# Performance work log

Hardware: AMD Instinct MI355X
Metric: run time of the kernel (lower is better)

Reference implementation:

```python
import jax, jax.numpy as jnp
import numpy as np

B, H, V, T = 32768, 1024, 9, 20
EOS = 8

def setup_inputs() -> dict:
    key = jax.random.key(0)
    ks = jax.random.split(key, 10)
    s_fc = 1.0 / np.sqrt(784)
    s_ih = 1.0 / np.sqrt(V)
    s_hh = 1.0 / np.sqrt(H)
    u = jax.random.uniform(ks[9], (T, B, V), jnp.float32, 1e-10, 1.0)
    return {
        "x": jax.random.normal(ks[0], (B, 784), jnp.float32),
        "tau": jnp.float32(1.0),
        "fc_w": jax.random.normal(ks[1], (H, 784), jnp.float32) * s_fc,
        "w_ih": jax.random.normal(ks[2], (3 * H, V), jnp.float32) * s_ih,
        "w_hh": jax.random.normal(ks[3], (3 * H, H), jnp.float32) * s_hh,
        "b_ih": jax.random.normal(ks[4], (3 * H,), jnp.float32) * s_hh,
        "b_hh": jax.random.normal(ks[5], (3 * H,), jnp.float32) * s_hh,
        "proj_w": jax.random.normal(ks[6], (V, H), jnp.float32) * s_hh,
        "proj_b": jax.random.normal(ks[7], (V,), jnp.float32) * s_hh,
        # standard Gumbel(0,1) noise, precomputed for all T steps
        "gumbel": -jnp.log(-jnp.log(u)),
    }


def reference(x, tau, fc_w, w_ih, w_hh, b_ih, b_hh, proj_w, proj_b, gumbel):
    # context = gelu(fc(x)); dropout is identity (eval mode)
    h0 = jax.nn.gelu(x @ fc_w.T, approximate=False)  # [B, H]
    b = x.shape[0]
    tok0 = jnp.zeros((b, V), x.dtype).at[:, 0].set(1.0)  # BOS one-hot

    def step(carry, g):
        h, tok, finished, lengths, t = carry
        gi = tok @ w_ih.T + b_ih            # [B, 3H]
        gh = h @ w_hh.T + b_hh              # [B, 3H]
        i_r, i_z, i_n = jnp.split(gi, 3, axis=-1)
        h_r, h_z, h_n = jnp.split(gh, 3, axis=-1)
        r = jax.nn.sigmoid(i_r + h_r)
        z = jax.nn.sigmoid(i_z + h_z)
        n = jnp.tanh(i_n + r * h_n)
        h_new = (1.0 - z) * n + z * h
        logits = h_new @ proj_w.T + proj_b  # [B, V]
        y_soft = jax.nn.softmax((logits + g) / tau, axis=-1)
        idx = jnp.argmax(y_soft, axis=-1)
        y_hard = jax.nn.one_hot(idx, V, dtype=y_soft.dtype)
        y = y_hard + y_soft - jax.lax.stop_gradient(y_soft)  # straight-through
        newly = (idx == EOS) & (~finished)
        lengths = jnp.where(newly, t + 1, lengths)
        finished = finished | newly
        return (h_new, y, finished, lengths, t + 1), y

    carry0 = (h0, tok0,
              jnp.zeros((b,), jnp.bool_),
              jnp.full((b,), T, jnp.int32),
              jnp.int32(0))
    (_, _, _, lengths, _), toks = jax.lax.scan(step, carry0, gumbel)
    message = jnp.transpose(toks, (1, 0, 2))  # [B, T, V]
    return message, lengths
```

## Files before the change

kernel.cpp:

```cpp
#include <hip/hip_runtime.h>
#include <math.h>

#define Bsz 32768
#define Hd  1024
#define Vn  9
#define Tn  20
#define EOSv 8
#define KFC 784
#define PLANE 33554432ull

typedef float f4 __attribute__((ext_vector_type(4)));
typedef float f32x16 __attribute__((ext_vector_type(16)));
typedef _Float16 h8 __attribute__((ext_vector_type(8)));
typedef unsigned short us4 __attribute__((ext_vector_type(4)));
typedef unsigned short us8v __attribute__((ext_vector_type(8)));

__device__ __forceinline__ unsigned short f16_rne(float x) {
    _Float16 h = (_Float16)x;
    return __builtin_bit_cast(unsigned short, h);
}
__device__ __forceinline__ float f16_val(unsigned short u) {
    return (float)__builtin_bit_cast(_Float16, u);
}
__device__ __forceinline__ void split2h(float x, unsigned short& p0, unsigned short& p1) {
    p0 = f16_rne(x);
    float r = x - f16_val(p0);
    p1 = f16_rne(r);
}
__device__ __forceinline__ int slotr(int r) { return r ^ ((r >> 3) & 3); }

__device__ __forceinline__ void gload16(const void* g, void* l) {
    __builtin_amdgcn_global_load_lds(
        (const __attribute__((address_space(1))) unsigned int*)g,
        (__attribute__((address_space(3))) unsigned int*)l, 16, 0, 0);
}

__global__ __launch_bounds__(256) void k_init(int* __restrict__ st,
                                              float* __restrict__ lenf) {
    int i = blockIdx.x * 256 + threadIdx.x;
    if (i < Bsz) { st[i] = 0; lenf[i] = (float)Tn; }
}

__global__ __launch_bounds__(256) void k_prep(const float* __restrict__ wih,
                                              const float* __restrict__ bih,
                                              float* __restrict__ giTab) {
    int i = blockIdx.x * 256 + threadIdx.x;
    int tk = i / 3072, n = i - tk * 3072;
    giTab[i] = wih[(size_t)n * Vn + tk] + bih[n];
}

__global__ __launch_bounds__(256) void k_prepB(const float* __restrict__ whh,
                                               unsigned short* __restrict__ wp) {
    int g = blockIdx.x * 256 + threadIdx.x;
    int lane = g & 63, u = g >> 6;
    int p = u & 1, kc = (u >> 1) & 63, ct = u >> 7;
    int col = ct * 32 + (lane & 31);
    int k = kc * 16 + (lane >> 5) * 8;
    const float* src = whh + (size_t)col * Hd + k;
    unsigned short v[8];
    #pragma unroll
    for (int i = 0; i < 8; ++i) {
        unsigned short s0, s1; split2h(src[i], s0, s1);
        v[i] = (p == 0) ? s0 : s1;
    }
    unsigned short* dst = wp + (size_t)u * 512 + lane * 8;
    us4 w0; w0[0]=v[0]; w0[1]=v[1]; w0[2]=v[2]; w0[3]=v[3];
    us4 w1; w1[0]=v[4]; w1[1]=v[5]; w1[2]=v[6]; w1[3]=v[7];
    *(us4*)dst = w0;
    *(us4*)(dst + 4) = w1;
}

__global__ __launch_bounds__(256) void k_fcP(const float* __restrict__ x,
                                             const float* __restrict__ fcw,
                                             float* __restrict__ h0,
                                             unsigned short* __restrict__ hp) {
    __shared__ float As[16][68];
    __shared__ float Ws[16][68];
    const int tid = threadIdx.x;
    const int tx = tid & 15, ty = tid >> 4;
    const int m0 = blockIdx.x * 64, n0 = blockIdx.y * 64;
    const int lrow = tid >> 2, lkc = (tid & 3) << 2;
    float acc[4][4] = {};
    for (int k0 = 0; k0 < KFC; k0 += 16) {
        f4 a = *(const f4*)(x   + (size_t)(m0 + lrow) * KFC + k0 + lkc);
        f4 w = *(const f4*)(fcw + (size_t)(n0 + lrow) * KFC + k0 + lkc);
        #pragma unroll
        for (int q = 0; q < 4; ++q) { As[lkc + q][lrow] = a[q]; Ws[lkc + q][lrow] = w[q]; }
        __syncthreads();
        #pragma unroll
        for (int kk = 0; kk < 16; ++kk) {
            f4 av = *(const f4*)&As[kk][ty * 4];
            f4 wv = *(const f4*)&Ws[kk][tx * 4];
            #pragma unroll
            for (int i = 0; i < 4; ++i)
                #pragma unroll
                for (int j = 0; j < 4; ++j)
                    acc[i][j] = fmaf(av[i], wv[j], acc[i][j]);
        }
        __syncthreads();
    }
    #pragma unroll
    for (int i = 0; i < 4; ++i) {
        int b = m0 + ty * 4 + i;
        int cb = n0 + tx * 4;
        f4 hv;
        us4 q0, q1;
        #pragma unroll
        for (int j = 0; j < 4; ++j) {
            float v = acc[i][j];
            float gl = 0.5f * v * (1.0f + erff(v * 0.70710678118654752f));
            hv[j] = gl;
            unsigned short s0, s1; split2h(gl, s0, s1);
            q0[j] = s0; q1[j] = s1;
        }
        *(f4*)&h0[(size_t)b * Hd + cb] = hv;
        *(us4*)&hp[0 * PLANE + (size_t)b * Hd + cb] = q0;
        *(us4*)&hp[1 * PLANE + (size_t)b * Hd + cb] = q1;
    }
}

__global__ __launch_bounds__(256, 3) void k_step(
        const unsigned short* __restrict__ hp, float* __restrict__ h,
        const unsigned short* __restrict__ wp, const float* __restrict__ bhh,
        const float* __restrict__ giTab, const int* __restrict__ st) {
    __shared__ unsigned short Asm[2][2 * 2 * 128 * 8];
    __shared__ unsigned short Bsm[2][12 * 512];
    const int tid = threadIdx.x;
    const int lane = tid & 63, wid = tid >> 6;
    const int wm = wid >> 1, wn = wid & 1;
    const int l31 = lane & 31, lh = lane >> 5;

    const int w = blockIdx.x;
    const int cg = (w & 7) * 2 + ((w >> 3) & 1);
    const int rb = w >> 4;
    const int m_blk = rb * 128;
    const int c0 = cg * 64;

    f32x16 acc[2][3];
    #pragma unroll
    for (int mt = 0; mt < 2; ++mt)
        #pragma unroll
        for (int g = 0; g < 3; ++g)
            #pragma unroll
            for (int e = 0; e < 16; ++e) acc[mt][g][e] = 0.0f;

    const int ar = tid >> 1;
    const int kh = tid & 1;
    const int wslot = slotr(ar);
    int rslot[2];
    #pragma unroll
    for (int mt = 0; mt < 2; ++mt) rslot[mt] = slotr(wm * 64 + mt * 32 + l31);

    us8v pa[2];
    auto load_a = [&](int s) {
        const size_t base = (size_t)(m_blk + ar) * Hd + (s << 4) + (kh << 3);
        pa[0] = *(const us8v*)&hp[0 * PLANE + base];
        pa[1] = *(const us8v*)&hp[1 * PLANE + base];
    };
    auto write_a = [&](int bufi) {
        *(us8v*)&Asm[bufi][((0 * 2 + kh) * 128 + wslot) * 8] = pa[0];
        *(us8v*)&Asm[bufi][((1 * 2 + kh) * 128 + wslot) * 8] = pa[1];
    };
    auto stage_b = [&](int s, int bufi) {
        #pragma unroll
        for (int q = 0; q < 3; ++q) {
            const int u = wid * 3 + q;
            const int ctl = u >> 1, p = u & 1;
            const int g = ctl >> 1, wnl = ctl & 1;
            const int ct = g * 32 + cg * 2 + wnl;
            const unsigned short* src = wp + ((size_t)(ct * 64 + s) * 2 + p) * 512 + lane * 8;
            gload16(src, &Bsm[bufi][u * 512]);
        }
    };

    stage_b(0, 0);
    load_a(0);
    write_a(0);
    load_a(1);
    __syncthreads();

    for (int s = 0; s < 64; ++s) {
        const int bi = s & 1;
        if (s < 63) {
            stage_b(s + 1, bi ^ 1);
            write_a(bi ^ 1);
        }
        if (s < 62) load_a(s + 2);
        h8 af[2][2];
        #pragma unroll
        for (int mt = 0; mt < 2; ++mt)
            #pragma unroll
            for (int p = 0; p < 2; ++p)
                af[mt][p] = *(const h8*)&Asm[bi][((p * 2 + lh) * 128 + rslot[mt]) * 8];
        #pragma unroll
        for (int g = 0; g < 3; ++g) {
            const int ub = (g * 2 + wn) * 2;
            h8 b0 = *(const h8*)&Bsm[bi][(ub + 0) * 512 + lane * 8];
            h8 b1 = *(const h8*)&Bsm[bi][(ub + 1) * 512 + lane * 8];
            #pragma unroll
            for (int mt = 0; mt < 2; ++mt) {
                f32x16 c = acc[mt][g];
                c = __builtin_amdgcn_mfma_f32_32x32x16_f16(af[mt][0], b1, c, 0, 0, 0);
                c = __builtin_amdgcn_mfma_f32_32x32x16_f16(af[mt][1], b0, c, 0, 0, 0);
                c = __builtin_amdgcn_mfma_f32_32x32x16_f16(af[mt][0], b0, c, 0, 0, 0);
                acc[mt][g] = c;
            }
        }
        __syncthreads();
    }

    const int col = c0 + wn * 32 + l31;
    const float bhr = bhh[col], bhz = bhh[Hd + col], bhn = bhh[2 * Hd + col];
    #pragma unroll
    for (int mt = 0; mt < 2; ++mt) {
        #pragma unroll
        for (int reg = 0; reg < 16; ++reg) {
            const int row = m_blk + wm * 64 + mt * 32 + 4 * lh + (reg & 3) + 8 * (reg >> 2);
            const int tk = st[row] & 15;
            const float* gi = giTab + tk * 3072;
            float rr = 1.0f / (1.0f + expf(-(gi[col] + acc[mt][0][reg] + bhr)));
            float zz = 1.0f / (1.0f + expf(-(gi[Hd + col] + acc[mt][1][reg] + bhz)));
            float nn = tanhf(gi[2 * Hd + col] + rr * (acc[mt][2][reg] + bhn));
            const size_t off = (size_t)row * Hd + col;
            float hold = h[off];
            h[off] = (1.0f - zz) * nn + zz * hold;
        }
    }
}

__global__ __launch_bounds__(256) void k_projP(const float* __restrict__ hnew,
        unsigned short* __restrict__ hp,
        const float* __restrict__ pw, const float* __restrict__ pb,
        const float* __restrict__ gum, const float* __restrict__ tau,
        float* __restrict__ msg, float* __restrict__ lenf,
        int* __restrict__ st, int t) {
    const int lane = threadIdx.x & 63;
    const int wv = threadIdx.x >> 6;
    const int b = blockIdx.x * 4 + wv;
    const float* hr = hnew + (size_t)b * Hd;
    float s[Vn] = {};
    float vals[16];
    #pragma unroll
    for (int c0 = 0; c0 < 16; c0 += 4) {
        f4 hv = *(const f4*)(hr + lane * 16 + c0);
        #pragma unroll
        for (int q = 0; q < 4; ++q) vals[c0 + q] = hv[q];
        #pragma unroll
        for (int v = 0; v < Vn; ++v) {
            f4 pv = *(const f4*)(pw + (size_t)v * Hd + lane * 16 + c0);
            #pragma unroll
            for (int q = 0; q < 4; ++q) s[v] = fmaf(hv[q], pv[q], s[v]);
        }
    }
    us8v o0[2], o1[2];
    #pragma unroll
    for (int hh = 0; hh < 2; ++hh)
        #pragma unroll
        for (int e = 0; e < 8; ++e) {
            unsigned short q0, q1;
            split2h(vals[hh * 8 + e], q0, q1);
            o0[hh][e] = q0; o1[hh][e] = q1;
        }
    size_t base = (size_t)b * Hd + lane * 16;
    #pragma unroll
    for (int hh = 0; hh < 2; ++hh) {
        *(us8v*)&hp[0 * PLANE + base + hh * 8] = o0[hh];
        *(us8v*)&hp[1 * PLANE + base + hh * 8] = o1[hh];
    }
    #pragma unroll
    for (int v = 0; v < Vn; ++v)
        #pragma unroll
        for (int off = 32; off > 0; off >>= 1)
            s[v] += __shfl_xor(s[v], off, 64);
    if (lane == 0) {
        const float tv = tau[0];
        float zv[Vn];
        #pragma unroll
        for (int v = 0; v < Vn; ++v)
            zv[v] = (s[v] + pb[v] + gum[(size_t)b * Vn + v]) / tv;
        int idx = 0; float m = zv[0];
        #pragma unroll
        for (int v = 1; v < Vn; ++v)
            if (zv[v] > m) { m = zv[v]; idx = v; }
        float* orow = msg + ((size_t)b * Tn + t) * Vn;
        #pragma unroll
        for (int v = 0; v < Vn; ++v) orow[v] = (v == idx) ? 1.0f : 0.0f;
        const int old = st[b];
        const int fn = old >> 4;
        st[b] = idx | (((fn != 0) || (idx == EOSv)) ? 16 : 0);
        if (idx == EOSv && fn == 0) lenf[b] = (float)(t + 1);
    }
}

extern "C" void kernel_launch(void* const* d_in, const int* in_sizes, int n_in,
                              void* d_out, int out_size, void* d_ws, size_t ws_size,
                              hipStream_t stream) {
    const float* x   = (const float*)d_in[0];
    const float* tau = (const float*)d_in[1];
    const float* fcw = (const float*)d_in[2];
    const float* wih = (const float*)d_in[3];
    const float* whh = (const float*)d_in[4];
    const float* bih = (const float*)d_in[5];
    const float* bhh = (const float*)d_in[6];
    const float* pw  = (const float*)d_in[7];
    const float* pb  = (const float*)d_in[8];
    const float* gum = (const float*)d_in[9];

    float* msg  = (float*)d_out;
    float* lenf = msg + (size_t)Bsz * Tn * Vn;

    char* ws = (char*)d_ws;
    float*          h     = (float*)ws;
    unsigned short* hp    = (unsigned short*)(ws + 134217728ull);
    unsigned short* wpb   = (unsigned short*)(ws + 268435456ull);
    float*          giTab = (float*)(ws + 281018368ull);
    int*            st    = (int*)  (ws + 281128960ull);

    k_init<<<Bsz / 256, 256, 0, stream>>>(st, lenf);
    k_prep<<<108, 256, 0, stream>>>(wih, bih, giTab);
    k_prepB<<<3072, 256, 0, stream>>>(whh, wpb);
    k_fcP<<<dim3(Bsz / 64, Hd / 64), 256, 0, stream>>>(x, fcw, h, hp);
    for (int t = 0; t < Tn; ++t) {
        k_step<<<4096, 256, 0, stream>>>(hp, h, wpb, bhh, giTab, st);
        k_projP<<<Bsz / 4, 256, 0, stream>>>(h, hp, pw, pb,
                                             gum + (size_t)t * Bsz * Vn,
                                             tau, msg, lenf, st, t);
    }
}
```

Baseline: 17.44 ms.

## Reshape GRU step tile to 64x128 with eight waves per block

Changes the recurrent GEMM block tile from 128 rows by 64 columns with four waves to 64 rows by 128 columns with eight waves, each wave holding one 32-row tile across three gates. This halves how many column groups re-read each h row from global memory, reducing activation traffic, while doubling weight staging per block. It also lowers per-wave accumulator registers but reduces MFMA work per shared-memory fragment load, and only half the threads load A.

```diff
diff --git a/kernel.cpp b/kernel.cpp
--- a/kernel.cpp
+++ b/kernel.cpp
@@ -119,92 +119,79 @@
     }
 }
 
-__global__ __launch_bounds__(256, 3) void k_step(
+__global__ __launch_bounds__(512) void k_step(
         const unsigned short* __restrict__ hp, float* __restrict__ h,
         const unsigned short* __restrict__ wp, const float* __restrict__ bhh,
         const float* __restrict__ giTab, const int* __restrict__ st) {
-    __shared__ unsigned short Asm[2][2 * 2 * 128 * 8];
-    __shared__ unsigned short Bsm[2][12 * 512];
+    __shared__ unsigned short Asm[2][2 * 2 * 64 * 8];
+    __shared__ unsigned short Bsm[2][24 * 512];
     const int tid = threadIdx.x;
     const int lane = tid & 63, wid = tid >> 6;
-    const int wm = wid >> 1, wn = wid & 1;
+    const int wm = wid >> 2, wn = wid & 3;
     const int l31 = lane & 31, lh = lane >> 5;
 
     const int w = blockIdx.x;
-    const int cg = (w & 7) * 2 + ((w >> 3) & 1);
-    const int rb = w >> 4;
-    const int m_blk = rb * 128;
-    const int c0 = cg * 64;
-
-    f32x16 acc[2][3];
-    #pragma unroll
-    for (int mt = 0; mt < 2; ++mt)
-        #pragma unroll
-        for (int g = 0; g < 3; ++g)
-            #pragma unroll
-            for (int e = 0; e < 16; ++e) acc[mt][g][e] = 0.0f;
-
-    const int ar = tid >> 1;
-    const int kh = tid & 1;
-    const int wslot = slotr(ar);
-    int rslot[2];
-    #pragma unroll
-    for (int mt = 0; mt < 2; ++mt) rslot[mt] = slotr(wm * 64 + mt * 32 + l31);
-
-    us8v pa[2];
+    const int cg = w & 7;
+    const int rb = w >> 3;
+    const int m_blk = rb * 64;
+    const int c0 = cg * 128;
+
+    f32x16 acc[3];
+    #pragma unroll
+    for (int g = 0; g < 3; ++g)
+        #pragma unroll
+        for (int e = 0; e < 16; ++e) acc[g][e] = 0.0f;
+
+    const int rslot = slotr(wm * 32 + l31);
+
+    const int ar = tid >> 2;
+    const int ap = (tid >> 1) & 1;
+    const int akh = tid & 1;
+    const int awslot = slotr(ar);
+
+    us8v pa;
     auto load_a = [&](int s) {
-        const size_t base = (size_t)(m_blk + ar) * Hd + (s << 4) + (kh << 3);
-        pa[0] = *(const us8v*)&hp[0 * PLANE + base];
-        pa[1] = *(const us8v*)&hp[1 * PLANE + base];
+        pa = *(const us8v*)&hp[(size_t)ap * PLANE + (size_t)(m_blk + ar) * Hd + (s << 4) + (akh << 3)];
     };
     auto write_a = [&](int bufi) {
-        *(us8v*)&Asm[bufi][((0 * 2 + kh) * 128 + wslot) * 8] = pa[0];
-        *(us8v*)&Asm[bufi][((1 * 2 + kh) * 128 + wslot) * 8] = pa[1];
+        *(us8v*)&Asm[bufi][((ap * 2 + akh) * 64 + awslot) * 8] = pa;
     };
     auto stage_b = [&](int s, int bufi) {
         #pragma unroll
         for (int q = 0; q < 3; ++q) {
             const int u = wid * 3 + q;
-            const int ctl = u >> 1, p = u & 1;
-            const int g = ctl >> 1, wnl = ctl & 1;
-            const int ct = g * 32 + cg * 2 + wnl;
+            const int wnl = u / 6;
+            const int rem = u - wnl * 6;
+            const int g = rem >> 1, p = rem & 1;
+            const int ct = g * 32 + cg * 4 + wnl;
             const unsigned short* src = wp + ((size_t)(ct * 64 + s) * 2 + p) * 512 + lane * 8;
             gload16(src, &Bsm[bufi][u * 512]);
         }
     };
 
     stage_b(0, 0);
-    load_a(0);
-    write_a(0);
-    load_a(1);
+    if (tid < 256) { load_a(0); write_a(0); load_a(1); }
     __syncthreads();
 
     for (int s = 0; s < 64; ++s) {
         const int bi = s & 1;
         if (s < 63) {
             stage_b(s + 1, bi ^ 1);
-            write_a(bi ^ 1);
-        }
-        if (s < 62) load_a(s + 2);
-        h8 af[2][2];
-        #pragma unroll
-        for (int mt = 0; mt < 2; ++mt)
-            #pragma unroll
-            for (int p = 0; p < 2; ++p)
-                af[mt][p] = *(const h8*)&Asm[bi][((p * 2 + lh) * 128 + rslot[mt]) * 8];
+            if (tid < 256) write_a(bi ^ 1);
+        }
+        if (s < 62 && tid < 256) load_a(s + 2);
+        h8 af0 = *(const h8*)&Asm[bi][((0 * 2 + lh) * 64 + rslot) * 8];
+        h8 af1 = *(const h8*)&Asm[bi][((1 * 2 + lh) * 64 + rslot) * 8];
         #pragma unroll
         for (int g = 0; g < 3; ++g) {
-            const int ub = (g * 2 + wn) * 2;
+            const int ub = wn * 6 + g * 2;
             h8 b0 = *(const h8*)&Bsm[bi][(ub + 0) * 512 + lane * 8];
             h8 b1 = *(const h8*)&Bsm[bi][(ub + 1) * 512 + lane * 8];
-            #pragma unroll
-            for (int mt = 0; mt < 2; ++mt) {
-                f32x16 c = acc[mt][g];
-                c = __builtin_amdgcn_mfma_f32_32x32x16_f16(af[mt][0], b1, c, 0, 0, 0);
-                c = __builtin_amdgcn_mfma_f32_32x32x16_f16(af[mt][1], b0, c, 0, 0, 0);
-                c = __builtin_amdgcn_mfma_f32_32x32x16_f16(af[mt][0], b0, c, 0, 0, 0);
-                acc[mt][g] = c;
-            }
+            f32x16 c = acc[g];
+            c = __builtin_amdgcn_mfma_f32_32x32x16_f16(af0, b1, c, 0, 0, 0);
+            c = __builtin_amdgcn_mfma_f32_32x32x16_f16(af1, b0, c, 0, 0, 0);
+            c = __builtin_amdgcn_mfma_f32_32x32x16_f16(af0, b0, c, 0, 0, 0);
+            acc[g] = c;
         }
         __syncthreads();
     }
@@ -212,19 +199,16 @@
     const int col = c0 + wn * 32 + l31;
     const float bhr = bhh[col], bhz = bhh[Hd + col], bhn = bhh[2 * Hd + col];
     #pragma unroll
-    for (int mt = 0; mt < 2; ++mt) {
-        #pragma unroll
-        for (int reg = 0; reg < 16; ++reg) {
-            const int row = m_blk + wm * 64 + mt * 32 + 4 * lh + (reg & 3) + 8 * (reg >> 2);
-            const int tk = st[row] & 15;
-            const float* gi = giTab + tk * 3072;
-            float rr = 1.0f / (1.0f + expf(-(gi[col] + acc[mt][0][reg] + bhr)));
-            float zz = 1.0f / (1.0f + expf(-(gi[Hd + col] + acc[mt][1][reg] + bhz)));
-            float nn = tanhf(gi[2 * Hd + col] + rr * (acc[mt][2][reg] + bhn));
-            const size_t off = (size_t)row * Hd + col;
-            float hold = h[off];
-            h[off] = (1.0f - zz) * nn + zz * hold;
-        }
+    for (int reg = 0; reg < 16; ++reg) {
+        const int row = m_blk + wm * 32 + 4 * lh + (reg & 3) + 8 * (reg >> 2);
+        const int tk = st[row] & 15;
+        const float* gi = giTab + tk * 3072;
+        float rr = 1.0f / (1.0f + expf(-(gi[col] + acc[0][reg] + bhr)));
+        float zz = 1.0f / (1.0f + expf(-(gi[Hd + col] + acc[1][reg] + bhz)));
+        float nn = tanhf(gi[2 * Hd + col] + rr * (acc[2][reg] + bhn));
+        const size_t off = (size_t)row * Hd + col;
+        float hold = h[off];
+        h[off] = (1.0f - zz) * nn + zz * hold;
     }
 }
 
@@ -321,7 +305,7 @@
     k_prepB<<<3072, 256, 0, stream>>>(whh, wpb);
     k_fcP<<<dim3(Bsz / 64, Hd / 64), 256, 0, stream>>>(x, fcw, h, hp);
     for (int t = 0; t < Tn; ++t) {
-        k_step<<<4096, 256, 0, stream>>>(hp, h, wpb, bhh, giTab, st);
+        k_step<<<4096, 512, 0, stream>>>(hp, h, wpb, bhh, giTab, st);
         k_projP<<<Bsz / 4, 256, 0, stream>>>(h, hp, pw, pb,
                                              gum + (size_t)t * Bsz * Vn,
                                              tau, msg, lenf, st, t);
```

After: 17.83 ms. 1.02x slower.
